# Kernel optimization log

Measured on AMD Instinct MI355X. Metric: run time of the kernel, lower is better.

Reference implementation:

```python
import jax, jax.numpy as jnp
import numpy as np

N_AGENTS = 64
_adj = np.ones((N_AGENTS, N_AGENTS)) - np.eye(N_AGENTS)
SEND_NP, RECV_NP = np.where(_adj)  # 4032 directed edges, no self-loops
N_EDGES = SEND_NP.shape[0]

D_NODE = 16
H = 64
D_OUT = 16
N_TYPES = 2
BATCH = 128


def _glorot(key, shape):
    fan_in, fan_out = shape[0], shape[1]
    lim = np.sqrt(6.0 / (fan_in + fan_out)).astype(np.float32)
    return jax.random.uniform(key, shape, jnp.float32, -lim, lim)


def setup_inputs() -> dict:
    key = jax.random.key(0)
    ks = jax.random.split(key, 16)
    inp = {
        "node_states": jax.random.normal(ks[0], (BATCH, N_AGENTS, 1, D_NODE), jnp.float32),
        "edge_types": jax.random.uniform(ks[1], (BATCH, N_EDGES, N_TYPES + 1, 1), jnp.float32),
        # edge encoder 0: MLP(32 -> 64 -> 64)
        "e0_w1": _glorot(ks[2], (2 * D_NODE, H)), "e0_b1": jnp.zeros((H,), jnp.float32),
        "e0_w2": _glorot(ks[3], (H, H)), "e0_b2": jnp.zeros((H,), jnp.float32),
        # edge encoder 1
        "e1_w1": _glorot(ks[4], (2 * D_NODE, H)), "e1_b1": jnp.zeros((H,), jnp.float32),
        "e1_w2": _glorot(ks[5], (H, H)), "e1_b2": jnp.zeros((H,), jnp.float32),
        # node decoder: MLP(16+64 -> 64 -> 16)
        "nd_w1": _glorot(ks[6], (D_NODE + H, H)), "nd_b1": jnp.zeros((H,), jnp.float32),
        "nd_w2": _glorot(ks[7], (H, D_OUT)), "nd_b2": jnp.zeros((D_OUT,), jnp.float32),
    }
    return inp


def _mlp2(x, w1, b1, w2, b2):
    h = jax.nn.relu(x @ w1 + b1)
    return jax.nn.relu(h @ w2 + b2)


def reference(node_states, edge_types,
              e0_w1, e0_b1, e0_w2, e0_b2,
              e1_w1, e1_b1, e1_w2, e1_b2,
              nd_w1, nd_b1, nd_w2, nd_b2):
    send = jnp.asarray(SEND_NP)
    recv = jnp.asarray(RECV_NP)
    # NodeAggregator: gather sender/receiver states to edges -> [B, E, 1, 2D]
    edge_msg = jnp.concatenate([node_states[:, send], node_states[:, recv]], axis=-1)
    # per-edge-type MLP encode, concat along axis 2 -> [B, E, T, H]
    enc0 = _mlp2(edge_msg, e0_w1, e0_b1, e0_w2, e0_b2)
    enc1 = _mlp2(edge_msg, e1_w1, e1_b1, e1_w2, e1_b2)
    encoded = jnp.concatenate([enc0, enc1], axis=2)
    # masked sum over edge types (skip type-0 'no edge') -> [B, E, 1, H]
    edge_msg_sum = jnp.sum(encoded * edge_types[:, :, 1:, :], axis=2, keepdims=True)
    # EdgeAggregator: scatter-sum edge messages to receiver nodes -> [B, N, 1, H]
    node_msg = jax.ops.segment_sum(
        edge_msg_sum.swapaxes(0, 1), recv, num_segments=N_AGENTS).swapaxes(0, 1)
    # decode
    node_state = jnp.concatenate([node_states, node_msg], axis=-1)  # [B, N, 1, D+H]
    return _mlp2(node_state, nd_w1, nd_b1, nd_w2, nd_b2)
```

## Files before the change

kernel.cpp:

```cpp
#include <hip/hip_runtime.h>


typedef __attribute__((ext_vector_type(8))) short bh8;
typedef __attribute__((ext_vector_type(4))) float fv4;

static __device__ __forceinline__ unsigned short f2bf(float f) {
  union { float f; unsigned u; } v; v.f = f;
  unsigned r = v.u + 0x7fffu + ((v.u >> 16) & 1u);
  return (unsigned short)(r >> 16);
}

__global__ __launch_bounds__(256) void prep_kernel(
    const float* __restrict__ ns,
    const float* __restrict__ e0w1, const float* __restrict__ e0b1,
    const float* __restrict__ e1w1, const float* __restrict__ e1b1,
    const float* __restrict__ e0w2, const float* __restrict__ e1w2,
    float* __restrict__ P0, float* __restrict__ Q0,
    float* __restrict__ P1, float* __restrict__ Q1,
    unsigned short* __restrict__ W2T)
{
  int bid = blockIdx.x, t = threadIdx.x;
  if (bid < 2048) {
    __shared__ float nsl[64];
    int b = bid >> 4, ng = bid & 15;
    if (t < 64) nsl[t] = ns[(b*64 + ng*4)*16 + t];
    __syncthreads();
    int n = ng*4 + (t >> 6), h = t & 63, li = (t >> 6)*16;
    float p0 = 0.f, q0 = 0.f, p1 = 0.f, q1 = 0.f;
#pragma unroll
    for (int k = 0; k < 16; ++k) {
      float x = nsl[li + k];
      p0 += x * e0w1[k*64 + h];
      q0 += x * e0w1[(16 + k)*64 + h];
      p1 += x * e1w1[k*64 + h];
      q1 += x * e1w1[(16 + k)*64 + h];
    }
    int row = b*64 + n;
    P0[row*64 + h] = p0;
    Q0[row*64 + h] = q0 + e0b1[h];
    P1[row*64 + h] = p1;
    Q1[row*64 + h] = q1 + e1b1[h];
  } else {
    int idx = (bid - 2048)*256 + t;
    int enc = idx / 4608, rem = idx % 4608;
    int n = rem / 72, kp = rem % 72;
    const float* w2 = enc ? e1w2 : e0w2;
    W2T[idx] = (kp < 64) ? f2bf(w2[kp*64 + n]) : (unsigned short)0;
  }
}

__global__ __launch_bounds__(256) void main_kernel(
    const float* __restrict__ ns, const float* __restrict__ et,
    const float* __restrict__ P0g, const float* __restrict__ Q0g,
    const float* __restrict__ P1g, const float* __restrict__ Q1g,
    const unsigned short* __restrict__ W2TW,
    const float* __restrict__ e0b2, const float* __restrict__ e1b2,
    const float* __restrict__ ndw1, const float* __restrict__ ndb1,
    const float* __restrict__ ndw2, const float* __restrict__ ndb2,
    float* __restrict__ out)
{
  __shared__ float Pl[2*64*68];
  __shared__ unsigned short W2T[2*64*72];
  __shared__ float Qb[2*8*64];
  __shared__ float ETl[2*8*64];
  __shared__ float B2l[128];
  __shared__ float MSG[8*64];
  __shared__ float NSR[8*16];

  int t = threadIdx.x;
  int b = blockIdx.x >> 3, rg = blockIdx.x & 7, r0 = rg*8;

  {
    const float4* src0 = (const float4*)(P0g + b*64*64);
    const float4* src1 = (const float4*)(P1g + b*64*64);
#pragma unroll
    for (int i = 0; i < 8; ++i) {
      int idx = t + i*256;
      int enc = idx >> 10, rem = idx & 1023;
      int s = rem >> 4, c4 = rem & 15;
      float4 v = enc ? src1[rem] : src0[rem];
      *(float4*)(Pl + enc*4352 + s*68 + c4*4) = v;
    }
  }
  {
    const unsigned* src = (const unsigned*)W2TW;
    unsigned* dst = (unsigned*)W2T;
#pragma unroll
    for (int i = 0; i < 18; ++i) dst[t + i*256] = src[t + i*256];
  }
#pragma unroll
  for (int i = 0; i < 4; ++i) {
    int idx = t + i*256;
    int enc = idx >> 9, rem = idx & 511;
    int rl = rem >> 6, k = rem & 63;
    const float* Q = enc ? Q1g : Q0g;
    Qb[idx] = Q[(b*64 + r0 + rl)*64 + k];
  }
#pragma unroll
  for (int i = 0; i < 4; ++i) {
    int idx = t + i*256;
    int enc = idx >> 9, rem = idx & 511;
    int rl = rem >> 6, s = rem & 63;
    int r = r0 + rl;
    float v = 0.f;
    if (s != r) {
      int e = s*63 + (r < s ? r : r - 1);
      v = et[(b*4032 + e)*3 + 1 + enc];
    }
    ETl[idx] = v;
  }
  if (t < 128) B2l[t] = (t >= 64) ? e1b2[t - 64] : e0b2[t];
  if (t < 128) { int rl = t >> 4; NSR[t] = ns[(b*64 + r0 + rl)*16 + (t & 15)]; }
  __syncthreads();

  int w = t >> 6, lane = t & 63, quad = lane >> 4, col = lane & 15;
  float msgacc[2][4] = {{0.f,0.f,0.f,0.f},{0.f,0.f,0.f,0.f}};

#pragma unroll
  for (int enc = 0; enc < 2; ++enc) {
    bh8 bf[4][2];
    float b2v[4];
#pragma unroll
    for (int nt = 0; nt < 4; ++nt) {
#pragma unroll
      for (int kk = 0; kk < 2; ++kk)
        bf[nt][kk] = *(const bh8*)(W2T + enc*4608 + (nt*16 + col)*72 + kk*32 + quad*8);
      b2v[nt] = B2l[enc*64 + nt*16 + col];
    }
#pragma unroll
    for (int rli = 0; rli < 2; ++rli) {
      int rl = w*2 + rli;
      const float* qrow = Qb + (enc*8 + rl)*64;
      float4 qa0 = *(const float4*)(qrow + quad*8);
      float4 qa1 = *(const float4*)(qrow + quad*8 + 4);
      float4 qb0 = *(const float4*)(qrow + 32 + quad*8);
      float4 qb1 = *(const float4*)(qrow + 32 + quad*8 + 4);
      const float* etrow = ETl + (enc*8 + rl)*64;
#pragma unroll
      for (int st = 0; st < 4; ++st) {
        const float* prow = Pl + enc*4352 + (st*16 + col)*68;
        float4 pa0 = *(const float4*)(prow + quad*8);
        float4 pa1 = *(const float4*)(prow + quad*8 + 4);
        float4 pb0 = *(const float4*)(prow + 32 + quad*8);
        float4 pb1 = *(const float4*)(prow + 32 + quad*8 + 4);
        bh8 a0, a1;
        a0[0] = (short)f2bf(fmaxf(pa0.x + qa0.x, 0.f));
        a0[1] = (short)f2bf(fmaxf(pa0.y + qa0.y, 0.f));
        a0[2] = (short)f2bf(fmaxf(pa0.z + qa0.z, 0.f));
        a0[3] = (short)f2bf(fmaxf(pa0.w + qa0.w, 0.f));
        a0[4] = (short)f2bf(fmaxf(pa1.x + qa1.x, 0.f));
        a0[5] = (short)f2bf(fmaxf(pa1.y + qa1.y, 0.f));
        a0[6] = (short)f2bf(fmaxf(pa1.z + qa1.z, 0.f));
        a0[7] = (short)f2bf(fmaxf(pa1.w + qa1.w, 0.f));
        a1[0] = (short)f2bf(fmaxf(pb0.x + qb0.x, 0.f));
        a1[1] = (short)f2bf(fmaxf(pb0.y + qb0.y, 0.f));
        a1[2] = (short)f2bf(fmaxf(pb0.z + qb0.z, 0.f));
        a1[3] = (short)f2bf(fmaxf(pb0.w + qb0.w, 0.f));
        a1[4] = (short)f2bf(fmaxf(pb1.x + qb1.x, 0.f));
        a1[5] = (short)f2bf(fmaxf(pb1.y + qb1.y, 0.f));
        a1[6] = (short)f2bf(fmaxf(pb1.z + qb1.z, 0.f));
        a1[7] = (short)f2bf(fmaxf(pb1.w + qb1.w, 0.f));
        float4 etv = *(const float4*)(etrow + st*16 + quad*4);
#pragma unroll
        for (int nt = 0; nt < 4; ++nt) {
          fv4 acc = {0.f, 0.f, 0.f, 0.f};
          acc = __builtin_amdgcn_mfma_f32_16x16x32_bf16(a0, bf[nt][0], acc, 0, 0, 0);
          acc = __builtin_amdgcn_mfma_f32_16x16x32_bf16(a1, bf[nt][1], acc, 0, 0, 0);
          float m = msgacc[rli][nt];
          m += etv.x * fmaxf(acc[0] + b2v[nt], 0.f);
          m += etv.y * fmaxf(acc[1] + b2v[nt], 0.f);
          m += etv.z * fmaxf(acc[2] + b2v[nt], 0.f);
          m += etv.w * fmaxf(acc[3] + b2v[nt], 0.f);
          msgacc[rli][nt] = m;
        }
      }
    }
  }
#pragma unroll
  for (int rli = 0; rli < 2; ++rli) {
#pragma unroll
    for (int nt = 0; nt < 4; ++nt) {
      float v = msgacc[rli][nt];
      v += __shfl_xor(v, 16);
      v += __shfl_xor(v, 32);
      if (lane < 16) MSG[(w*2 + rli)*64 + nt*16 + lane] = v;
    }
  }
  __syncthreads();

  float* HD = Pl;
#pragma unroll
  for (int pass = 0; pass < 2; ++pass) {
    int idx = pass*256 + t;
    int rl = idx >> 6, j = idx & 63;
    float acc = ndb1[j];
    const float* x0 = NSR + rl*16;
#pragma unroll
    for (int i = 0; i < 16; ++i) acc += x0[i] * ndw1[i*64 + j];
    const float* mrow = MSG + rl*64;
    for (int i = 0; i < 64; ++i) acc += mrow[i] * ndw1[(16 + i)*64 + j];
    HD[idx] = fmaxf(acc, 0.f);
  }
  __syncthreads();
  if (t < 128) {
    int rl = t >> 4, o = t & 15;
    float acc = ndb2[o];
#pragma unroll
    for (int j = 0; j < 64; ++j) acc += HD[rl*64 + j] * ndw2[j*16 + o];
    out[(b*64 + r0 + rl)*16 + o] = fmaxf(acc, 0.f);
  }
}

extern "C" void kernel_launch(void* const* d_in, const int* in_sizes, int n_in,
                              void* d_out, int out_size, void* d_ws, size_t ws_size,
                              hipStream_t stream) {
  const float* ns   = (const float*)d_in[0];
  const float* et   = (const float*)d_in[1];
  const float* e0w1 = (const float*)d_in[2];
  const float* e0b1 = (const float*)d_in[3];
  const float* e0w2 = (const float*)d_in[4];
  const float* e0b2 = (const float*)d_in[5];
  const float* e1w1 = (const float*)d_in[6];
  const float* e1b1 = (const float*)d_in[7];
  const float* e1w2 = (const float*)d_in[8];
  const float* e1b2 = (const float*)d_in[9];
  const float* ndw1 = (const float*)d_in[10];
  const float* ndb1 = (const float*)d_in[11];
  const float* ndw2 = (const float*)d_in[12];
  const float* ndb2 = (const float*)d_in[13];

  float* P0 = (float*)d_ws;
  float* Q0 = P0 + 524288;
  float* P1 = Q0 + 524288;
  float* Q1 = P1 + 524288;
  unsigned short* W2TW = (unsigned short*)(Q1 + 524288);

  prep_kernel<<<2084, 256, 0, stream>>>(ns, e0w1, e0b1, e1w1, e1b1, e0w2, e1w2,
                                        P0, Q0, P1, Q1, W2TW);
  main_kernel<<<1024, 256, 0, stream>>>(ns, et, P0, Q0, P1, Q1, W2TW,
                                        e0b2, e1b2, ndw1, ndb1, ndw2, ndb2,
                                        (float*)d_out);
}
```

Before: 135.1 us.

## Fuse prep into main kernel, recompute P/Q per block and load W2 directly

Removes the separate prep kernel and its global workspace round-trip. Each block now recomputes the first-layer P projections for all 64 senders of its batch, plus Q for its 8 receivers, from node states in shared memory. W2 is converted to bf16 fragments straight from global memory instead of a pre-transposed buffer. It also switches to the packed bf16 conversion intrinsics and sets a launch-bounds occupancy hint. This trades one launch and the workspace traffic for about 8x redundant P computation per batch and strided global reads of W2.

```diff
diff --git a/kernel.cpp b/kernel.cpp
--- a/kernel.cpp
+++ b/kernel.cpp
@@ -1,104 +1,71 @@
 #include <hip/hip_runtime.h>
+#include <hip/hip_bf16.h>
 
 
 typedef __attribute__((ext_vector_type(8))) short bh8;
 typedef __attribute__((ext_vector_type(4))) float fv4;
 
-static __device__ __forceinline__ unsigned short f2bf(float f) {
-  union { float f; unsigned u; } v; v.f = f;
-  unsigned r = v.u + 0x7fffu + ((v.u >> 16) & 1u);
-  return (unsigned short)(r >> 16);
-}
-
-__global__ __launch_bounds__(256) void prep_kernel(
-    const float* __restrict__ ns,
+union AB { bh8 v; __hip_bfloat162 h[4]; };
+
+__global__ __launch_bounds__(256, 3) void fused_kernel(
+    const float* __restrict__ ns, const float* __restrict__ et,
     const float* __restrict__ e0w1, const float* __restrict__ e0b1,
+    const float* __restrict__ e0w2, const float* __restrict__ e0b2,
     const float* __restrict__ e1w1, const float* __restrict__ e1b1,
-    const float* __restrict__ e0w2, const float* __restrict__ e1w2,
-    float* __restrict__ P0, float* __restrict__ Q0,
-    float* __restrict__ P1, float* __restrict__ Q1,
-    unsigned short* __restrict__ W2T)
-{
-  int bid = blockIdx.x, t = threadIdx.x;
-  if (bid < 2048) {
-    __shared__ float nsl[64];
-    int b = bid >> 4, ng = bid & 15;
-    if (t < 64) nsl[t] = ns[(b*64 + ng*4)*16 + t];
-    __syncthreads();
-    int n = ng*4 + (t >> 6), h = t & 63, li = (t >> 6)*16;
-    float p0 = 0.f, q0 = 0.f, p1 = 0.f, q1 = 0.f;
-#pragma unroll
-    for (int k = 0; k < 16; ++k) {
-      float x = nsl[li + k];
-      p0 += x * e0w1[k*64 + h];
-      q0 += x * e0w1[(16 + k)*64 + h];
-      p1 += x * e1w1[k*64 + h];
-      q1 += x * e1w1[(16 + k)*64 + h];
-    }
-    int row = b*64 + n;
-    P0[row*64 + h] = p0;
-    Q0[row*64 + h] = q0 + e0b1[h];
-    P1[row*64 + h] = p1;
-    Q1[row*64 + h] = q1 + e1b1[h];
-  } else {
-    int idx = (bid - 2048)*256 + t;
-    int enc = idx / 4608, rem = idx % 4608;
-    int n = rem / 72, kp = rem % 72;
-    const float* w2 = enc ? e1w2 : e0w2;
-    W2T[idx] = (kp < 64) ? f2bf(w2[kp*64 + n]) : (unsigned short)0;
-  }
-}
-
-__global__ __launch_bounds__(256) void main_kernel(
-    const float* __restrict__ ns, const float* __restrict__ et,
-    const float* __restrict__ P0g, const float* __restrict__ Q0g,
-    const float* __restrict__ P1g, const float* __restrict__ Q1g,
-    const unsigned short* __restrict__ W2TW,
-    const float* __restrict__ e0b2, const float* __restrict__ e1b2,
+    const float* __restrict__ e1w2, const float* __restrict__ e1b2,
     const float* __restrict__ ndw1, const float* __restrict__ ndb1,
     const float* __restrict__ ndw2, const float* __restrict__ ndb2,
     float* __restrict__ out)
 {
+  __shared__ float NSl[64*16];
   __shared__ float Pl[2*64*68];
-  __shared__ unsigned short W2T[2*64*72];
   __shared__ float Qb[2*8*64];
   __shared__ float ETl[2*8*64];
-  __shared__ float B2l[128];
   __shared__ float MSG[8*64];
-  __shared__ float NSR[8*16];
 
   int t = threadIdx.x;
   int b = blockIdx.x >> 3, rg = blockIdx.x & 7, r0 = rg*8;
+  int w = t >> 6, lane = t & 63, quad = lane >> 4, col = lane & 15;
+
+  ((float4*)NSl)[t] = ((const float4*)(ns + b*1024))[t];
+  __syncthreads();
 
   {
-    const float4* src0 = (const float4*)(P0g + b*64*64);
-    const float4* src1 = (const float4*)(P1g + b*64*64);
-#pragma unroll
-    for (int i = 0; i < 8; ++i) {
-      int idx = t + i*256;
-      int enc = idx >> 10, rem = idx & 1023;
-      int s = rem >> 4, c4 = rem & 15;
-      float4 v = enc ? src1[rem] : src0[rem];
-      *(float4*)(Pl + enc*4352 + s*68 + c4*4) = v;
-    }
-  }
-  {
-    const unsigned* src = (const unsigned*)W2TW;
-    unsigned* dst = (unsigned*)W2T;
-#pragma unroll
-    for (int i = 0; i < 18; ++i) dst[t + i*256] = src[t + i*256];
+    int h = lane;
+#pragma unroll
+    for (int enc = 0; enc < 2; ++enc) {
+      const float* w1 = enc ? e1w1 : e0w1;
+      float wc[16];
+#pragma unroll
+      for (int k = 0; k < 16; ++k) wc[k] = w1[k*64 + h];
+      float* pdst = Pl + enc*4352;
+#pragma unroll
+      for (int si = 0; si < 16; ++si) {
+        int s = w*16 + si;
+        const float* x = NSl + s*16;
+        float acc = 0.f;
+#pragma unroll
+        for (int k = 0; k < 16; ++k) acc += wc[k] * x[k];
+        pdst[s*68 + h] = acc;
+      }
+    }
   }
 #pragma unroll
   for (int i = 0; i < 4; ++i) {
-    int idx = t + i*256;
+    int idx = i*256 + t;
     int enc = idx >> 9, rem = idx & 511;
-    int rl = rem >> 6, k = rem & 63;
-    const float* Q = enc ? Q1g : Q0g;
-    Qb[idx] = Q[(b*64 + r0 + rl)*64 + k];
+    int rl = rem >> 6, h = rem & 63;
+    const float* w1 = enc ? e1w1 : e0w1;
+    const float* b1 = enc ? e1b1 : e0b1;
+    const float* x = NSl + (r0 + rl)*16;
+    float acc = b1[h];
+#pragma unroll
+    for (int k = 0; k < 16; ++k) acc += w1[(16 + k)*64 + h] * x[k];
+    Qb[idx] = acc;
   }
 #pragma unroll
   for (int i = 0; i < 4; ++i) {
-    int idx = t + i*256;
+    int idx = i*256 + t;
     int enc = idx >> 9, rem = idx & 511;
     int rl = rem >> 6, s = rem & 63;
     int r = r0 + rl;
@@ -109,23 +76,31 @@
     }
     ETl[idx] = v;
   }
-  if (t < 128) B2l[t] = (t >= 64) ? e1b2[t - 64] : e0b2[t];
-  if (t < 128) { int rl = t >> 4; NSR[t] = ns[(b*64 + r0 + rl)*16 + (t & 15)]; }
-  __syncthreads();
-
-  int w = t >> 6, lane = t & 63, quad = lane >> 4, col = lane & 15;
+  __syncthreads();
+
   float msgacc[2][4] = {{0.f,0.f,0.f,0.f},{0.f,0.f,0.f,0.f}};
 
 #pragma unroll
   for (int enc = 0; enc < 2; ++enc) {
+    const float* w2 = enc ? e1w2 : e0w2;
+    const float* b2 = enc ? e1b2 : e0b2;
     bh8 bf[4][2];
     float b2v[4];
 #pragma unroll
     for (int nt = 0; nt < 4; ++nt) {
 #pragma unroll
-      for (int kk = 0; kk < 2; ++kk)
-        bf[nt][kk] = *(const bh8*)(W2T + enc*4608 + (nt*16 + col)*72 + kk*32 + quad*8);
-      b2v[nt] = B2l[enc*64 + nt*16 + col];
+      for (int kk = 0; kk < 2; ++kk) {
+        const float* base = w2 + (kk*32 + quad*8)*64 + nt*16 + col;
+        float f0 = base[0*64], f1 = base[1*64], f2 = base[2*64], f3 = base[3*64];
+        float f4 = base[4*64], f5 = base[5*64], f6 = base[6*64], f7 = base[7*64];
+        AB bb;
+        bb.h[0] = __float22bfloat162_rn(make_float2(f0, f1));
+        bb.h[1] = __float22bfloat162_rn(make_float2(f2, f3));
+        bb.h[2] = __float22bfloat162_rn(make_float2(f4, f5));
+        bb.h[3] = __float22bfloat162_rn(make_float2(f6, f7));
+        bf[nt][kk] = bb.v;
+      }
+      b2v[nt] = b2[nt*16 + col];
     }
 #pragma unroll
     for (int rli = 0; rli < 2; ++rli) {
@@ -143,29 +118,21 @@
         float4 pa1 = *(const float4*)(prow + quad*8 + 4);
         float4 pb0 = *(const float4*)(prow + 32 + quad*8);
         float4 pb1 = *(const float4*)(prow + 32 + quad*8 + 4);
-        bh8 a0, a1;
-        a0[0] = (short)f2bf(fmaxf(pa0.x + qa0.x, 0.f));
-        a0[1] = (short)f2bf(fmaxf(pa0.y + qa0.y, 0.f));
-        a0[2] = (short)f2bf(fmaxf(pa0.z + qa0.z, 0.f));
-        a0[3] = (short)f2bf(fmaxf(pa0.w + qa0.w, 0.f));
-        a0[4] = (short)f2bf(fmaxf(pa1.x + qa1.x, 0.f));
-        a0[5] = (short)f2bf(fmaxf(pa1.y + qa1.y, 0.f));
-        a0[6] = (short)f2bf(fmaxf(pa1.z + qa1.z, 0.f));
-        a0[7] = (short)f2bf(fmaxf(pa1.w + qa1.w, 0.f));
-        a1[0] = (short)f2bf(fmaxf(pb0.x + qb0.x, 0.f));
-        a1[1] = (short)f2bf(fmaxf(pb0.y + qb0.y, 0.f));
-        a1[2] = (short)f2bf(fmaxf(pb0.z + qb0.z, 0.f));
-        a1[3] = (short)f2bf(fmaxf(pb0.w + qb0.w, 0.f));
-        a1[4] = (short)f2bf(fmaxf(pb1.x + qb1.x, 0.f));
-        a1[5] = (short)f2bf(fmaxf(pb1.y + qb1.y, 0.f));
-        a1[6] = (short)f2bf(fmaxf(pb1.z + qb1.z, 0.f));
-        a1[7] = (short)f2bf(fmaxf(pb1.w + qb1.w, 0.f));
+        AB a0, a1;
+        a0.h[0] = __float22bfloat162_rn(make_float2(fmaxf(pa0.x + qa0.x, 0.f), fmaxf(pa0.y + qa0.y, 0.f)));
+        a0.h[1] = __float22bfloat162_rn(make_float2(fmaxf(pa0.z + qa0.z, 0.f), fmaxf(pa0.w + qa0.w, 0.f)));
+        a0.h[2] = __float22bfloat162_rn(make_float2(fmaxf(pa1.x + qa1.x, 0.f), fmaxf(pa1.y + qa1.y, 0.f)));
+        a0.h[3] = __float22bfloat162_rn(make_float2(fmaxf(pa1.z + qa1.z, 0.f), fmaxf(pa1.w + qa1.w, 0.f)));
+        a1.h[0] = __float22bfloat162_rn(make_float2(fmaxf(pb0.x + qb0.x, 0.f), fmaxf(pb0.y + qb0.y, 0.f)));
+        a1.h[1] = __float22bfloat162_rn(make_float2(fmaxf(pb0.z + qb0.z, 0.f), fmaxf(pb0.w + qb0.w, 0.f)));
+        a1.h[2] = __float22bfloat162_rn(make_float2(fmaxf(pb1.x + qb1.x, 0.f), fmaxf(pb1.y + qb1.y, 0.f)));
+        a1.h[3] = __float22bfloat162_rn(make_float2(fmaxf(pb1.z + qb1.z, 0.f), fmaxf(pb1.w + qb1.w, 0.f)));
         float4 etv = *(const float4*)(etrow + st*16 + quad*4);
 #pragma unroll
         for (int nt = 0; nt < 4; ++nt) {
           fv4 acc = {0.f, 0.f, 0.f, 0.f};
-          acc = __builtin_amdgcn_mfma_f32_16x16x32_bf16(a0, bf[nt][0], acc, 0, 0, 0);
-          acc = __builtin_amdgcn_mfma_f32_16x16x32_bf16(a1, bf[nt][1], acc, 0, 0, 0);
+          acc = __builtin_amdgcn_mfma_f32_16x16x32_bf16(a0.v, bf[nt][0], acc, 0, 0, 0);
+          acc = __builtin_amdgcn_mfma_f32_16x16x32_bf16(a1.v, bf[nt][1], acc, 0, 0, 0);
           float m = msgacc[rli][nt];
           m += etv.x * fmaxf(acc[0] + b2v[nt], 0.f);
           m += etv.y * fmaxf(acc[1] + b2v[nt], 0.f);
@@ -194,7 +161,7 @@
     int idx = pass*256 + t;
     int rl = idx >> 6, j = idx & 63;
     float acc = ndb1[j];
-    const float* x0 = NSR + rl*16;
+    const float* x0 = NSl + (r0 + rl)*16;
 #pragma unroll
     for (int i = 0; i < 16; ++i) acc += x0[i] * ndw1[i*64 + j];
     const float* mrow = MSG + rl*64;
@@ -229,15 +196,9 @@
   const float* ndw2 = (const float*)d_in[12];
   const float* ndb2 = (const float*)d_in[13];
 
-  float* P0 = (float*)d_ws;
-  float* Q0 = P0 + 524288;
-  float* P1 = Q0 + 524288;
-  float* Q1 = P1 + 524288;
-  unsigned short* W2TW = (unsigned short*)(Q1 + 524288);
-
-  prep_kernel<<<2084, 256, 0, stream>>>(ns, e0w1, e0b1, e1w1, e1b1, e0w2, e1w2,
-                                        P0, Q0, P1, Q1, W2TW);
-  main_kernel<<<1024, 256, 0, stream>>>(ns, et, P0, Q0, P1, Q1, W2TW,
-                                        e0b2, e1b2, ndw1, ndb1, ndw2, ndb2,
-                                        (float*)d_out);
+  fused_kernel<<<1024, 256, 0, stream>>>(ns, et,
+                                         e0w1, e0b1, e0w2, e0b2,
+                                         e1w1, e1b1, e1w2, e1b2,
+                                         ndw1, ndb1, ndw2, ndb2,
+                                         (float*)d_out);
 }
```

Result: slower. 178.1 us (+31.9%).
